# Optimization experiments

Hardware: AMD Instinct MI355X
Metric: run time of the kernel (lower is better)

## Reference

```python
import jax, jax.numpy as jnp
import numpy as np

B, Q, V, T = 96, 96, 197, 77   # image batch, text batch, visual tokens, text tokens
DV, DT, E = 768, 768, 512      # visual_size, textual_size, embed_size


def l2norm(x):
    # F.normalize(t, dim=-1, p=2) with eps=1e-12
    n = jnp.linalg.norm(x, axis=-1, keepdims=True)
    return x / jnp.maximum(n, 1e-12)


def setup_inputs() -> dict:
    key = jax.random.key(0)
    ks = jax.random.split(key, 12)
    sv = 1.0 / np.sqrt(DV).astype(np.float32)
    st = 1.0 / np.sqrt(DT).astype(np.float32)
    return {
        "visual_cls": jax.random.normal(ks[0], (B, DV), jnp.float32),
        "visual_tokens": jax.random.normal(ks[1], (B, V, DV), jnp.float32),
        "textual_cls": jax.random.normal(ks[2], (Q, DT), jnp.float32),
        "textual_tokens": jax.random.normal(ks[3], (Q, T, DT), jnp.float32),
        "Wv_cls": jax.random.normal(ks[4], (E, DV), jnp.float32) * sv,
        "bv_cls": jnp.zeros((E,), jnp.float32),
        "Wt_cls": jax.random.normal(ks[5], (E, DT), jnp.float32) * st,
        "bt_cls": jnp.zeros((E,), jnp.float32),
        "Wv_tok": jax.random.normal(ks[6], (E, DV), jnp.float32) * sv,
        "bv_tok": jnp.zeros((E,), jnp.float32),
        "Wt_tok": jax.random.normal(ks[7], (E, DT), jnp.float32) * st,
        "bt_tok": jnp.zeros((E,), jnp.float32),
        "text_length": jax.random.randint(ks[8], (Q,), 5, T + 1, jnp.int32),
    }


def reference(visual_cls, visual_tokens, textual_cls, textual_tokens,
              Wv_cls, bv_cls, Wt_cls, bt_cls,
              Wv_tok, bv_tok, Wt_tok, bt_tok, text_length):
    # Linear projections (torch nn.Linear: y = x @ W.T + b)
    v_cls = visual_cls @ Wv_cls.T + bv_cls            # [b, e]
    t_cls = textual_cls @ Wt_cls.T + bt_cls           # [q, e]
    v_tok = l2norm(jnp.einsum('bvd,ed->bve', visual_tokens, Wv_tok) + bv_tok)   # [b, v, e]
    t_tok = l2norm(jnp.einsum('qtd,ed->qte', textual_tokens, Wt_tok) + bt_tok)  # [q, t, e]

    # valid-token mask from caption lengths: mask[q, t]
    mask = (jnp.arange(T)[None, :] < text_length[:, None]).astype(v_tok.dtype)

    # fine-grained token similarity: [b, q, v, t], masked on text tokens
    logits = jnp.einsum('bve,qte->bqvt', v_tok, t_tok) * mask[None, :, None, :]

    text_sum = mask.sum(-1)                           # [q]
    t2v = logits.max(axis=2).sum(axis=2) / text_sum[None, :]   # [b, q]
    v2t = logits.max(axis=3).sum(axis=2) / V                   # [b, q]
    return (v_cls, t_cls, t2v, v2t)
```

## Files before the change

kernel.cpp:

```cpp
#include <hip/hip_runtime.h>

#define NB 96
#define NQ 96
#define NV 197
#define NT 77
#define DK 768
#define DE 512

typedef __attribute__((ext_vector_type(8))) short s16x8;
typedef __attribute__((ext_vector_type(4))) float f32x4;
typedef long long i64;

__device__ __forceinline__ unsigned short f2bf(float f) {
  union { float f; unsigned int u; } v; v.f = f;
  unsigned int u = v.u;
  unsigned int r = u + 0x7fffu + ((u >> 16) & 1u);
  return (unsigned short)(r >> 16);
}

__device__ __forceinline__ unsigned int pack2bf(float a, float b) {
  return (unsigned int)f2bf(a) | ((unsigned int)f2bf(b) << 16);
}

__device__ __forceinline__ unsigned char f2fp8(float x) {
  union { float f; unsigned u; } v; v.f = x;
  unsigned s = (v.u >> 24) & 0x80;
  v.u &= 0x7FFFFFFFu;
  if (v.f < 0.015625f) {
    int q = __float2int_rn(v.f * 512.0f);
    return (unsigned char)(s | (unsigned)q);
  }
  if (v.f >= 464.0f) return (unsigned char)(s | 0x7E);
  int e8 = (int)((v.u >> 23) & 0xFF) - 120;
  unsigned m = v.u & 0x7FFFFFu;
  unsigned t = ((unsigned)e8 << 3) | (m >> 20);
  unsigned r = m & 0xFFFFFu;
  t += (r > 0x80000u) || ((r == 0x80000u) && (t & 1u));
  if (t > 0x7Eu) t = 0x7Eu;
  return (unsigned char)(s | t);
}

#define GL16(gp, lp, off)                                                \
  __builtin_amdgcn_global_load_lds(                                      \
      (const __attribute__((address_space(1))) void*)(gp),               \
      (__attribute__((address_space(3))) void*)(lp), 16, (off), 0)

#define VM_DRAIN() asm volatile("s_waitcnt vmcnt(0) lgkmcnt(0)" ::: "memory")

__global__ __launch_bounds__(256) void prep_kernel(
    const float* __restrict__ Wv_tok, unsigned short* __restrict__ Wvb,
    const float* __restrict__ Wt_tok, unsigned short* __restrict__ Wtb,
    const float* __restrict__ visual_cls, const float* __restrict__ Wv_cls,
    const float* __restrict__ bv_cls, float* __restrict__ v_cls_o,
    const float* __restrict__ textual_cls, const float* __restrict__ Wt_cls,
    const float* __restrict__ bt_cls, float* __restrict__ t_cls_o) {
  __shared__ float xs[DK];
  const int blk = blockIdx.x;
  const int tid = threadIdx.x;

  if (blk < 768) {
    const float* src = (blk < 384) ? Wv_tok : Wt_tok;
    unsigned short* dst = (blk < 384) ? Wvb : Wtb;
    int i = ((blk < 384) ? blk : (blk - 384)) * 256 + tid;
    float4 x = ((const float4*)src)[i];
    ushort4 h;
    h.x = f2bf(x.x); h.y = f2bf(x.y); h.z = f2bf(x.z); h.w = f2bf(x.w);
    ((ushort4*)dst)[i] = h;
    return;
  }
  const int is_t = (blk >= 864);
  const int row = blk - (is_t ? 864 : 768);
  const float* X = is_t ? textual_cls : visual_cls;
  const float* W = is_t ? Wt_cls : Wv_cls;
  const float* bias = is_t ? bt_cls : bv_cls;
  float* out = is_t ? t_cls_o : v_cls_o;

  const float* xr = X + (long)row * DK;
  for (int i = tid; i < DK; i += 256) xs[i] = xr[i];
  __syncthreads();
  for (int c = tid; c < DE; c += 256) {
    const float* wr = W + (long)c * DK;
    float s = 0.f;
    #pragma unroll 4
    for (int k = 0; k < DK; k += 4) {
      float4 w4 = *(const float4*)(wr + k);
      s += xs[k] * w4.x + xs[k + 1] * w4.y + xs[k + 2] * w4.z + xs[k + 3] * w4.w;
    }
    out[(long)row * DE + c] = s + bias[c];
  }
}

__global__ __launch_bounds__(256, 2) void proj_norm_kernel(
    const float* __restrict__ Xv, const unsigned short* __restrict__ Wvb,
    const float* __restrict__ bv, unsigned char* __restrict__ Yv,
    const float* __restrict__ Xt, const unsigned short* __restrict__ Wtb,
    const float* __restrict__ bt, unsigned char* __restrict__ Yt) {
  __shared__ __align__(16) unsigned short Ws[512 * 64];
  __shared__ __align__(16) unsigned short Xs[64 * 64];
  __shared__ float ssq_lds[4][64];

  const int blk = blockIdx.x;
  const int is_t = (blk >= 296);
  const float* X = is_t ? Xt : Xv;
  const unsigned short* Wb = is_t ? Wtb : Wvb;
  const float* bias = is_t ? bt : bv;
  unsigned char* Y = is_t ? Yt : Yv;
  const int M = is_t ? (NQ * NT) : (NB * NV);
  const long row0 = (long)(is_t ? (blk - 296) : blk) * 64;

  const int tid = threadIdx.x;
  const int wave = tid >> 6;
  const int lane = tid & 63;
  const int l15 = lane & 15;
  const int quad = lane >> 4;

  const int sub = lane >> 3;
  const int swz = ((lane & 7) ^ sub) << 3;
  const unsigned short* pw_base = Wb + (long)(wave * 8 + sub) * DK + swz;

  const int xrow_a = tid >> 3;
  const int xrow_b = xrow_a + 32;
  const int xs8 = tid & 7;
  long gra = row0 + xrow_a; if (gra > M - 1) gra = M - 1;
  long grb = row0 + xrow_b; if (grb > M - 1) grb = M - 1;
  const float* px_a = X + gra * DK + xs8 * 8;
  const float* px_b = X + grb * DK + xs8 * 8;
  const int xaddr_a = (xrow_a << 6) + ((xs8 ^ (xrow_a & 7)) << 3);
  const int xaddr_b = (xrow_b << 6) + ((xs8 ^ (xrow_b & 7)) << 3);

  f32x4 acc[4][8];
  #pragma unroll
  for (int m = 0; m < 4; ++m)
    #pragma unroll
    for (int n = 0; n < 8; ++n)
      acc[m][n] = (f32x4){0.f, 0.f, 0.f, 0.f};

  for (int kc = 0; kc < DK; kc += 64) {
    __syncthreads();
    {
      float4 x0 = *(const float4*)(px_a);
      float4 x1 = *(const float4*)(px_a + 4);
      uint4 h;
      h.x = pack2bf(x0.x, x0.y); h.y = pack2bf(x0.z, x0.w);
      h.z = pack2bf(x1.x, x1.y); h.w = pack2bf(x1.z, x1.w);
      *(uint4*)(&Xs[xaddr_a]) = h;
      x0 = *(const float4*)(px_b);
      x1 = *(const float4*)(px_b + 4);
      h.x = pack2bf(x0.x, x0.y); h.y = pack2bf(x0.z, x0.w);
      h.z = pack2bf(x1.x, x1.y); h.w = pack2bf(x1.z, x1.w);
      *(uint4*)(&Xs[xaddr_b]) = h;
      px_a += 64; px_b += 64;
    }
    {
      const unsigned short* pw = pw_base;
      #pragma unroll
      for (int j = 0; j < 16; ++j) {
        GL16(pw, &Ws[(j * 4 + wave) << 9], 0);
        pw += 32 * DK;
      }
      pw_base += 64;
    }
    VM_DRAIN();
    __syncthreads();
    #pragma unroll
    for (int ks = 0; ks < 2; ++ks) {
      s16x8 af[4];
      #pragma unroll
      for (int mi = 0; mi < 4; ++mi) {
        int arow = mi * 16 + l15;
        af[mi] = *(const s16x8*)&Xs[(arow << 6) + ((((ks << 2) + quad) ^ (arow & 7)) << 3)];
      }
      #pragma unroll
      for (int nt = 0; nt < 8; ++nt) {
        int wrow = wave * 128 + nt * 16 + l15;
        s16x8 bfr = *(const s16x8*)&Ws[(wrow << 6) + ((((ks << 2) + quad) ^ (wrow & 7)) << 3)];
        #pragma unroll
        for (int mi = 0; mi < 4; ++mi)
          acc[mi][nt] = __builtin_amdgcn_mfma_f32_16x16x32_bf16(af[mi], bfr, acc[mi][nt], 0, 0, 0);
      }
    }
  }

  #pragma unroll
  for (int nt = 0; nt < 8; ++nt) {
    float bc = bias[wave * 128 + nt * 16 + l15];
    #pragma unroll
    for (int mi = 0; mi < 4; ++mi) {
      acc[mi][nt].x += bc; acc[mi][nt].y += bc; acc[mi][nt].z += bc; acc[mi][nt].w += bc;
    }
  }

  #pragma unroll
  for (int mi = 0; mi < 4; ++mi)
    #pragma unroll
    for (int r = 0; r < 4; ++r) {
      float t = 0.f;
      #pragma unroll
      for (int nt = 0; nt < 8; ++nt) { float v = acc[mi][nt][r]; t += v * v; }
      t += __shfl_xor(t, 1);
      t += __shfl_xor(t, 2);
      t += __shfl_xor(t, 4);
      t += __shfl_xor(t, 8);
      if (l15 == 0) ssq_lds[wave][mi * 16 + quad * 4 + r] = t;
    }
  __syncthreads();

  #pragma unroll
  for (int mi = 0; mi < 4; ++mi) {
    #pragma unroll
    for (int r = 0; r < 4; ++r) {
      int rr = mi * 16 + quad * 4 + r;
      float tot = ssq_lds[0][rr] + ssq_lds[1][rr] + ssq_lds[2][rr] + ssq_lds[3][rr];
      float scale = (tot > 0.f) ? (1.f / fmaxf(sqrtf(tot), 1e-12f)) : 0.f;
      long grow = row0 + rr;
      if (grow < M) {
        #pragma unroll
        for (int nt = 0; nt < 8; ++nt) {
          int col = wave * 128 + nt * 16 + l15;
          Y[grow * DE + col] = f2fp8(acc[mi][nt][r] * scale);
        }
      }
    }
  }
}

__global__ __launch_bounds__(256, 2) void score_kernel(
    const unsigned char* __restrict__ Yv, const unsigned char* __restrict__ Yt,
    const int* __restrict__ tlen, float* __restrict__ t2v, float* __restrict__ v2t) {
  __shared__ __align__(16) unsigned char pool[79232];
  float (*colbuf)[160] = (float(*)[160])pool;
  float (*rowsum_lds)[2] = (float(*)[2])(pool + 2560);

  const int tid = threadIdx.x;
  const int wave = tid >> 6;
  const int lane = tid & 63;
  const int l15 = lane & 15;
  const int quad = lane >> 4;

  const int idx = blockIdx.x;
  const int x = idx & 7;
  const int g = idx >> 3;
  const int qi = g / 12;
  const int bslot = g - qi * 12;
  const int b = bslot * 8 + x;
  const int q0 = qi * 2;

  const unsigned char* Ab = Yv + (long)b * (NV * DE);
  const unsigned char* Bb = Yt + (long)q0 * (NT * DE);

  if (tid < 96) *(int*)(pool + 78848 + tid * 4) = 0;

  const unsigned char* pa[4];
  #pragma unroll
  for (int i = 0; i < 4; ++i) {
    int row = (wave + (i << 2)) * 16 + l15;
    if (row > NV - 1) row = NV - 1;
    pa[i] = Ab + row * DE + (quad << 3);
  }

  const int ul = lane >> 3;
  const int slot = lane & 7;
  #pragma unroll
  for (int cc = 0; cc < 2; ++cc) {
    const int c = wave * 2 + cc;
    const unsigned char* cb = Bb + c * 64;
    #pragma unroll
    for (int s = 0; s < 10; ++s) {
      int u = (s < 9) ? (s * 8 + ul) : (69 + ul);
      int r = u * 2 + (slot & 1);
      int h = (r >= NT);
      int t = r - NT * h;
      const unsigned char* gp = cb + ((long)h * NT + t) * DE + (((slot >> 1) ^ (u & 3)) << 4);
      int sbase = (s < 9) ? (s << 10) : 8832;
      GL16(gp, pool + c * 9856 + sbase, 0);
    }
  }

  const int qh = quad >> 1;
  const int q8 = (quad & 1) << 3;
  int boff[10];
  #pragma unroll
  for (int nt = 0; nt < 10; ++nt) {
    int brow = nt * 16 + l15;
    int u = brow >> 1;
    boff[nt] = (u << 7) + ((qh ^ (u & 3)) << 5) + ((brow & 1) << 4) + q8;
  }

  f32x4 acc[4][10];
  #pragma unroll
  for (int i = 0; i < 4; ++i)
    #pragma unroll
    for (int nt = 0; nt < 10; ++nt)
      acc[i][nt] = (f32x4){0.f, 0.f, 0.f, 0.f};

  auto do_compute = [&](int c, const i64* af) {
    const int base = c * 9856;
    #pragma unroll
    for (int ks = 0; ks < 2; ++ks) {
      const int kx = ks ? 64 : 0;
      i64 bf[10];
      #pragma unroll
      for (int nt = 0; nt < 10; ++nt)
        bf[nt] = *(const i64*)&pool[base + (boff[nt] ^ kx)];
      __builtin_amdgcn_s_setprio(1);
      #pragma unroll
      for (int i = 0; i < 4; ++i) {
        if (wave + (i << 2) < 13) {
          #pragma unroll
          for (int nt = 0; nt < 10; ++nt)
            acc[i][nt] = __builtin_amdgcn_mfma_f32_16x16x32_fp8_fp8(
                af[i * 2 + ks], bf[nt], acc[i][nt], 0, 0, 0);
        }
      }
      __builtin_amdgcn_s_setprio(0);
    }
  };

#define LOADA(c, af)                                                     \
  {                                                                      \
    _Pragma("unroll")                                                    \
    for (int i = 0; i < 4; ++i) {                                        \
      if (wave + (i << 2) < 13) {                                        \
        af[i * 2]     = *(const i64*)(pa[i] + (c) * 64);                 \
        af[i * 2 + 1] = *(const i64*)(pa[i] + (c) * 64 + 32);            \
      }                                                                  \
    }                                                                    \
  }

  i64 af0[8] = {0, 0, 0, 0, 0, 0, 0, 0};
  i64 af1[8] = {0, 0, 0, 0, 0, 0, 0, 0};

  LOADA(0, af0)
  VM_DRAIN();
  __syncthreads();

  LOADA(1, af1)  do_compute(0, af0);
  LOADA(2, af0)  do_compute(1, af1);
  LOADA(3, af1)  do_compute(2, af0);
  LOADA(4, af0)  do_compute(3, af1);
  LOADA(5, af1)  do_compute(4, af0);
  LOADA(6, af0)  do_compute(5, af1);
  LOADA(7, af1)  do_compute(6, af0);
  do_compute(7, af1);

#undef LOADA

  __syncthreads();

  const int len0 = tlen[q0];
  const int len1 = tlen[q0 + 1];

  #pragma unroll
  for (int nt = 0; nt < 10; ++nt) {
    float m = -1e30f;
    #pragma unroll
    for (int i = 0; i < 4; ++i) {
      int mt = wave + (i << 2);
      if (mt < 13) {
        int mbase = mt * 16 + quad * 4;
        #pragma unroll
        for (int r = 0; r < 4; ++r)
          if (mbase + r < NV) m = fmaxf(m, acc[i][nt][r]);
      }
    }
    m = fmaxf(m, __shfl_xor(m, 16));
    m = fmaxf(m, __shfl_xor(m, 32));
    if (lane < 16) colbuf[wave][nt * 16 + l15] = m;
  }

  float psum[2] = {0.f, 0.f};
  #pragma unroll
  for (int i = 0; i < 4; ++i) {
    int mt = wave + (i << 2);
    if (mt < 13) {
      int mbase = mt * 16 + quad * 4;
      #pragma unroll
      for (int r = 0; r < 4; ++r) {
        float rm = -1e30f;
        #pragma unroll
        for (int nt = 0; nt < 5; ++nt) {
          int gcol = nt * 16 + l15;
          if (gcol < len0) rm = fmaxf(rm, acc[i][nt][r]);
        }
        rm = fmaxf(rm, __shfl_xor(rm, 1));
        rm = fmaxf(rm, __shfl_xor(rm, 2));
        rm = fmaxf(rm, __shfl_xor(rm, 4));
        rm = fmaxf(rm, __shfl_xor(rm, 8));
        if (len0 < NT) rm = fmaxf(rm, 0.f);
        if (l15 == 0 && (mbase + r) < NV) psum[0] += rm;
        float rm1 = -1e30f;
        #pragma unroll
        for (int nt = 4; nt < 10; ++nt) {
          int gcol = nt * 16 + l15;
          if (gcol >= NT && gcol < NT + len1) rm1 = fmaxf(rm1, acc[i][nt][r]);
        }
        rm1 = fmaxf(rm1, __shfl_xor(rm1, 1));
        rm1 = fmaxf(rm1, __shfl_xor(rm1, 2));
        rm1 = fmaxf(rm1, __shfl_xor(rm1, 4));
        rm1 = fmaxf(rm1, __shfl_xor(rm1, 8));
        if (len1 < NT) rm1 = fmaxf(rm1, 0.f);
        if (l15 == 0 && (mbase + r) < NV) psum[1] += rm1;
      }
    }
  }
  psum[0] += __shfl_xor(psum[0], 16);
  psum[0] += __shfl_xor(psum[0], 32);
  psum[1] += __shfl_xor(psum[1], 16);
  psum[1] += __shfl_xor(psum[1], 32);
  if (lane == 0) { rowsum_lds[wave][0] = psum[0]; rowsum_lds[wave][1] = psum[1]; }
  __syncthreads();

  if (wave < 2) {
    int q = q0 + wave;
    int len = wave ? len1 : len0;
    int cbase = wave * NT;
    float ssum = 0.f;
    for (int c = lane; c < NT; c += 64) {
      if (c < len) {
        float m = fmaxf(fmaxf(colbuf[0][cbase + c], colbuf[1][cbase + c]),
                        fmaxf(colbuf[2][cbase + c], colbuf[3][cbase + c]));
        ssum += m;
      }
    }
    ssum += __shfl_xor(ssum, 1);
    ssum += __shfl_xor(ssum, 2);
    ssum += __shfl_xor(ssum, 4);
    ssum += __shfl_xor(ssum, 8);
    ssum += __shfl_xor(ssum, 16);
    ssum += __shfl_xor(ssum, 32);
    if (lane == 0) {
      float rs = rowsum_lds[0][wave] + rowsum_lds[1][wave] +
                 rowsum_lds[2][wave] + rowsum_lds[3][wave];
      t2v[b * NQ + q] = ssum / (float)len;
      v2t[b * NQ + q] = rs / (float)NV;
    }
  }
}

extern "C" void kernel_launch(void* const* d_in, const int* in_sizes, int n_in,
                              void* d_out, int out_size, void* d_ws, size_t ws_size,
                              hipStream_t stream) {
  (void)in_sizes; (void)n_in; (void)out_size; (void)ws_size;
  const float* visual_cls     = (const float*)d_in[0];
  const float* visual_tokens  = (const float*)d_in[1];
  const float* textual_cls    = (const float*)d_in[2];
  const float* textual_tokens = (const float*)d_in[3];
  const float* Wv_cls = (const float*)d_in[4];
  const float* bv_cls = (const float*)d_in[5];
  const float* Wt_cls = (const float*)d_in[6];
  const float* bt_cls = (const float*)d_in[7];
  const float* Wv_tok = (const float*)d_in[8];
  const float* bv_tok = (const float*)d_in[9];
  const float* Wt_tok = (const float*)d_in[10];
  const float* bt_tok = (const float*)d_in[11];
  const int* text_length = (const int*)d_in[12];

  float* out = (float*)d_out;
  float* v_cls_o = out;
  float* t_cls_o = out + 49152;
  float* t2v_o   = out + 98304;
  float* v2t_o   = out + 107520;

  char* ws = (char*)d_ws;
  unsigned short* Wvb = (unsigned short*)(ws);
  unsigned short* Wtb = (unsigned short*)(ws + 786432);
  unsigned char*  Yv  = (unsigned char*)(ws + 1572864);
  unsigned char*  Yt  = (unsigned char*)(ws + 1572864 + 9683968);

  prep_kernel<<<960, 256, 0, stream>>>(
      Wv_tok, Wvb, Wt_tok, Wtb,
      visual_cls, Wv_cls, bv_cls, v_cls_o,
      textual_cls, Wt_cls, bt_cls, t_cls_o);

  proj_norm_kernel<<<412, 256, 0, stream>>>(
      visual_tokens, Wvb, bv_tok, Yv,
      textual_tokens, Wtb, bt_tok, Yt);

  score_kernel<<<(NB * NQ) / 2, 256, 0, stream>>>(Yv, Yt, text_length, t2v_o, v2t_o);
}
```

Baseline: 405.0 us.

## Double-buffer per-wave W tiles and load X directly into registers in projection GEMM

Restructures the projection GEMM main loop. Each wave now owns private double-buffered LDS slices of its W rows, and the X activations are loaded straight from global into MFMA A-fragments in registers. This removes the block-wide __syncthreads and the shared X staging. Loads for chunk c+1 are issued before the MFMAs of chunk c, and s_setprio is raised around the MFMAs to overlap memory with compute. The cost is more VGPRs for the prefetched X and B fragments, a 32-wide K step with more iterations, and X read redundantly by each of the four waves.

```diff
diff --git a/kernel.cpp b/kernel.cpp
--- a/kernel.cpp
+++ b/kernel.cpp
@@ -46,6 +46,7 @@
       (__attribute__((address_space(3))) void*)(lp), 16, (off), 0)
 
 #define VM_DRAIN() asm volatile("s_waitcnt vmcnt(0) lgkmcnt(0)" ::: "memory")
+#define VMWAIT0()  asm volatile("s_waitcnt vmcnt(0)" ::: "memory")
 
 __global__ __launch_bounds__(256) void prep_kernel(
     const float* __restrict__ Wv_tok, unsigned short* __restrict__ Wvb,
@@ -95,8 +96,7 @@
     const float* __restrict__ bv, unsigned char* __restrict__ Yv,
     const float* __restrict__ Xt, const unsigned short* __restrict__ Wtb,
     const float* __restrict__ bt, unsigned char* __restrict__ Yt) {
-  __shared__ __align__(16) unsigned short Ws[512 * 64];
-  __shared__ __align__(16) unsigned short Xs[64 * 64];
+  __shared__ __align__(16) unsigned short Wl[4][2][4096];
   __shared__ float ssq_lds[4][64];
 
   const int blk = blockIdx.x;
@@ -114,19 +114,30 @@
   const int l15 = lane & 15;
   const int quad = lane >> 4;
 
-  const int sub = lane >> 3;
-  const int swz = ((lane & 7) ^ sub) << 3;
-  const unsigned short* pw_base = Wb + (long)(wave * 8 + sub) * DK + swz;
-
-  const int xrow_a = tid >> 3;
-  const int xrow_b = xrow_a + 32;
-  const int xs8 = tid & 7;
-  long gra = row0 + xrow_a; if (gra > M - 1) gra = M - 1;
-  long grb = row0 + xrow_b; if (grb > M - 1) grb = M - 1;
-  const float* px_a = X + gra * DK + xs8 * 8;
-  const float* px_b = X + grb * DK + xs8 * 8;
-  const int xaddr_a = (xrow_a << 6) + ((xs8 ^ (xrow_a & 7)) << 3);
-  const int xaddr_b = (xrow_b << 6) + ((xs8 ^ (xrow_b & 7)) << 3);
+  const int ul = lane >> 3;
+  const int slot = lane & 7;
+  const unsigned short* pw[8];
+  #pragma unroll
+  for (int s = 0; s < 8; ++s) {
+    int wrow = wave * 128 + s * 16 + ul * 2 + (slot & 1);
+    pw[s] = Wb + (long)wrow * DK + (((slot >> 1) ^ (ul & 3)) << 3);
+  }
+
+  const float* px[4];
+  #pragma unroll
+  for (int mi = 0; mi < 4; ++mi) {
+    long gr = row0 + mi * 16 + l15;
+    if (gr > M - 1) gr = M - 1;
+    px[mi] = X + gr * DK + quad * 8;
+  }
+
+  int boff[8];
+  #pragma unroll
+  for (int nt = 0; nt < 8; ++nt) {
+    int row = nt * 16 + l15;
+    int u = row >> 1;
+    boff[nt] = (u << 7) + (((((quad) ^ (u & 3)) << 1) | (row & 1)) << 4);
+  }
 
   f32x4 acc[4][8];
   #pragma unroll
@@ -135,51 +146,66 @@
     for (int n = 0; n < 8; ++n)
       acc[m][n] = (f32x4){0.f, 0.f, 0.f, 0.f};
 
-  for (int kc = 0; kc < DK; kc += 64) {
-    __syncthreads();
-    {
-      float4 x0 = *(const float4*)(px_a);
-      float4 x1 = *(const float4*)(px_a + 4);
-      uint4 h;
-      h.x = pack2bf(x0.x, x0.y); h.y = pack2bf(x0.z, x0.w);
-      h.z = pack2bf(x1.x, x1.y); h.w = pack2bf(x1.z, x1.w);
-      *(uint4*)(&Xs[xaddr_a]) = h;
-      x0 = *(const float4*)(px_b);
-      x1 = *(const float4*)(px_b + 4);
-      h.x = pack2bf(x0.x, x0.y); h.y = pack2bf(x0.z, x0.w);
-      h.z = pack2bf(x1.x, x1.y); h.w = pack2bf(x1.z, x1.w);
-      *(uint4*)(&Xs[xaddr_b]) = h;
-      px_a += 64; px_b += 64;
-    }
-    {
-      const unsigned short* pw = pw_base;
+  float4 xra[4], xrb[4];
+  s16x8 af[4];
+
+#define PSTAGE(p, c)                                                     \
+  {                                                                      \
+    _Pragma("unroll")                                                    \
+    for (int s = 0; s < 8; ++s)                                          \
+      GL16(pw[s] + (c) * 32, &Wl[wave][p][s * 512], 0);                  \
+  }
+
+#define PLOADX(c)                                                        \
+  {                                                                      \
+    _Pragma("unroll")                                                    \
+    for (int mi = 0; mi < 4; ++mi) {                                     \
+      xra[mi] = *(const float4*)(px[mi] + (c) * 32);                     \
+      xrb[mi] = *(const float4*)(px[mi] + (c) * 32 + 4);                 \
+    }                                                                    \
+  }
+
+#define PCVT()                                                           \
+  {                                                                      \
+    _Pragma("unroll")                                                    \
+    for (int mi = 0; mi < 4; ++mi) {                                     \
+      union { uint4 u; s16x8 v; } cv;                                    \
+      cv.u.x = pack2bf(xra[mi].x, xra[mi].y);                            \
+      cv.u.y = pack2bf(xra[mi].z, xra[mi].w);                            \
+      cv.u.z = pack2bf(xrb[mi].x, xrb[mi].y);                            \
+      cv.u.w = pack2bf(xrb[mi].z, xrb[mi].w);                            \
+      af[mi] = cv.v;                                                     \
+    }                                                                    \
+  }
+
+  PSTAGE(0, 0)
+  PLOADX(0)
+
+  #pragma unroll 2
+  for (int c = 0; c < 24; ++c) {
+    const int p = c & 1;
+    VMWAIT0();
+    PCVT();
+    if (c < 23) {
+      PSTAGE(1 - p, c + 1);
+      PLOADX(c + 1);
+    }
+    s16x8 bfr[8];
+    #pragma unroll
+    for (int nt = 0; nt < 8; ++nt)
+      bfr[nt] = *(const s16x8*)((const char*)&Wl[wave][p][0] + boff[nt]);
+    __builtin_amdgcn_s_setprio(1);
+    #pragma unroll
+    for (int nt = 0; nt < 8; ++nt)
       #pragma unroll
-      for (int j = 0; j < 16; ++j) {
-        GL16(pw, &Ws[(j * 4 + wave) << 9], 0);
-        pw += 32 * DK;
-      }
-      pw_base += 64;
-    }
-    VM_DRAIN();
-    __syncthreads();
-    #pragma unroll
-    for (int ks = 0; ks < 2; ++ks) {
-      s16x8 af[4];
-      #pragma unroll
-      for (int mi = 0; mi < 4; ++mi) {
-        int arow = mi * 16 + l15;
-        af[mi] = *(const s16x8*)&Xs[(arow << 6) + ((((ks << 2) + quad) ^ (arow & 7)) << 3)];
-      }
-      #pragma unroll
-      for (int nt = 0; nt < 8; ++nt) {
-        int wrow = wave * 128 + nt * 16 + l15;
-        s16x8 bfr = *(const s16x8*)&Ws[(wrow << 6) + ((((ks << 2) + quad) ^ (wrow & 7)) << 3)];
-        #pragma unroll
-        for (int mi = 0; mi < 4; ++mi)
-          acc[mi][nt] = __builtin_amdgcn_mfma_f32_16x16x32_bf16(af[mi], bfr, acc[mi][nt], 0, 0, 0);
-      }
-    }
-  }
+      for (int mi = 0; mi < 4; ++mi)
+        acc[mi][nt] = __builtin_amdgcn_mfma_f32_16x16x32_bf16(af[mi], bfr[nt], acc[mi][nt], 0, 0, 0);
+    __builtin_amdgcn_s_setprio(0);
+  }
+
+#undef PSTAGE
+#undef PLOADX
+#undef PCVT
 
   #pragma unroll
   for (int nt = 0; nt < 8; ++nt) {
```

New measurement: 445.5 us. 1.1x slower.
